# Kernel optimization log

Measured on AMD Instinct MI355X. Metric: run time of the kernel, lower is better.

The kernel has to match this reference:

```python
import jax, jax.numpy as jnp
import numpy as np

E = 256
H = 8
DK = E // H


def setup_inputs() -> dict:
    key = jax.random.key(0)
    ks = jax.random.split(key, 16)
    B, NA, NB = 2, 2048, 2048
    x_a = jax.random.normal(ks[0], (B, NA, E), dtype=jnp.float32)
    x_b = jax.random.normal(ks[1], (B, NB, E), dtype=jnp.float32)
    s = 1.0 / np.sqrt(E)  # kaiming-normal-ish scale
    inp = {"x_a": x_a, "x_b": x_b}
    names = ["wq", "wk_a", "wk_b", "wv_a", "wv_b", "w"]
    for i, n in enumerate(names):
        inp[n + "_w"] = jax.random.normal(ks[2 + 2 * i], (E, E), dtype=jnp.float32) * s
        inp[n + "_b"] = jax.random.normal(ks[3 + 2 * i], (E,), dtype=jnp.float32) * 0.01
    return inp


def _linear(x, w, b):
    # torch nn.Linear: y = x @ w.T + b
    return jnp.einsum('bne,fe->bnf', x, w) + b


def _heads(x):
    # [B, N, E] -> [B, H, N, DK]
    B, N, _ = x.shape
    return x.reshape(B, N, H, DK).transpose(0, 2, 1, 3)


def reference(x_a, x_b, wq_w, wq_b, wk_a_w, wk_a_b, wk_b_w, wk_b_b,
              wv_a_w, wv_a_b, wv_b_w, wv_b_b, w_w, w_b):
    B, NA, _ = x_a.shape
    q = _heads(_linear(x_a, wq_w, wq_b))          # [B,H,NA,DK]
    k_a = _heads(_linear(x_a, wk_a_w, wk_a_b))    # [B,H,NA,DK]
    v_a = _heads(_linear(x_a, wv_a_w, wv_a_b))
    k_b = _heads(_linear(x_b, wk_b_w, wk_b_b))    # [B,H,NB,DK]
    v_b = _heads(_linear(x_b, wv_b_w, wv_b_b))
    k = jnp.concatenate([k_a, k_b], axis=2)       # [B,H,NA+NB,DK]
    v = jnp.concatenate([v_a, v_b], axis=2)
    scores = jnp.einsum('bhqd,bhkd->bhqk', q, k) / jnp.sqrt(jnp.float32(DK))
    p = jax.nn.softmax(scores, axis=-1)           # [B,H,NA,NA+NB]
    z = jnp.einsum('bhqk,bhkd->bhqd', p, v)       # [B,H,NA,DK]
    z = z.transpose(0, 2, 1, 3).reshape(B, NA, E)
    out = _linear(z, w_w, w_b) + x_a
    return out
```

## Files before the change

### kernel.cpp

```cpp
#include <hip/hip_runtime.h>
#include <cstdint>

typedef short bf16x8 __attribute__((ext_vector_type(8)));
typedef float f32x4 __attribute__((ext_vector_type(4)));
typedef unsigned short u16;
typedef unsigned int u32;

#define DEVI static __device__ __forceinline__


DEVI u16 f2bf(float f) {
  u32 x = __builtin_bit_cast(u32, f);
  x += 0x7fffu + ((x >> 16) & 1u);
  return (u16)(x >> 16);
}

DEVI u32 pack_bf2(float lo, float hi) {
  return (u32)f2bf(lo) | ((u32)f2bf(hi) << 16);
}

DEVI u32 cvt_pk_bf16(float lo, float hi) {
  u32 r;
  asm("v_cvt_pk_bf16_f32 %0, %1, %2" : "=v"(r) : "v"(lo), "v"(hi));
  return r;
}

DEVI f32x4 mfma16(bf16x8 a, bf16x8 b, f32x4 c) {
  return __builtin_amdgcn_mfma_f32_16x16x32_bf16(a, b, c, 0, 0, 0);
}

DEVI void load_lds16(const void* g, void* l) {
  __builtin_amdgcn_global_load_lds(
      (const __attribute__((address_space(1))) u32*)g,
      (__attribute__((address_space(3))) u32*)l, 16, 0, 0);
}

#define CSCALE 0.2550351f

DEVI int rho(int k) {
  return ((k >> 5) << 5) | (((k >> 2) & 1) << 4) | (((k >> 3) & 3) << 2) | (k & 3);
}

__global__ __launch_bounds__(256) void convert_kernel(
    const float* __restrict__ xa, const float* __restrict__ xb,
    const float* __restrict__ w0, const float* __restrict__ w1,
    const float* __restrict__ w2, const float* __restrict__ w3,
    const float* __restrict__ w4, const float* __restrict__ w5,
    u16* __restrict__ dst) {
  int i = (int)(blockIdx.x * 256u + threadIdx.x) * 8;
  const float* s;
  if (i < 1048576) {
    s = xa + i;
  } else if (i < 2097152) {
    s = xb + (i - 1048576);
  } else {
    int t = i - 2097152;
    int j = t >> 16, o = t & 65535;
    s = (j == 0 ? w0 : j == 1 ? w1 : j == 2 ? w2 : j == 3 ? w3 : j == 4 ? w4 : w5) + o;
  }
  float4 a = *(const float4*)s;
  float4 b = *(const float4*)(s + 4);
  uint4 o4;
  o4.x = pack_bf2(a.x, a.y);
  o4.y = pack_bf2(a.z, a.w);
  o4.z = pack_bf2(b.x, b.y);
  o4.w = pack_bf2(b.z, b.w);
  *(uint4*)(dst + i) = o4;
}

__global__ __launch_bounds__(256) void proj_kernel(
    const u16* __restrict__ xa_bf, const u16* __restrict__ xb_bf,
    const u16* __restrict__ wbase,
    const float* __restrict__ b0, const float* __restrict__ b1,
    const float* __restrict__ b2, const float* __restrict__ b3,
    const float* __restrict__ b4,
    u16* __restrict__ Qo, u16* __restrict__ Ko, u16* __restrict__ Vo) {
  int job = blockIdx.z;
  const u16* A = (job <= 2) ? xa_bf : xb_bf;
  const u16* W = wbase + job * 65536;
  const float* bias = job == 0 ? b0 : job == 1 ? b1 : job == 2 ? b2 : job == 3 ? b3 : b4;
  int mode = (job == 0) ? 0 : (job == 1 || job == 3) ? 1 : 2;
  int soff = (job >= 3) ? 2048 : 0;

  int tid = threadIdx.x, wid = tid >> 6, lane = tid & 63, g = lane >> 4, c = lane & 15;
  int m0 = blockIdx.x * 64, n0 = blockIdx.y * 64;
  const u16* Ap = A + (size_t)(m0 + wid * 16 + c) * 256 + g * 8;
  const u16* Wp = W + (n0 + c) * 256 + g * 8;
  f32x4 acc[4] = {};
#pragma unroll
  for (int kk = 0; kk < 256; kk += 32) {
    bf16x8 af = *(const bf16x8*)(Ap + kk);
#pragma unroll
    for (int nt = 0; nt < 4; ++nt) {
      bf16x8 bfr = *(const bf16x8*)(Wp + nt * 4096 + kk);
      acc[nt] = mfma16(af, bfr, acc[nt]);
    }
  }
#pragma unroll
  for (int nt = 0; nt < 4; ++nt) {
    int f = n0 + nt * 16 + c;
    float bv = bias[f];
    int h = f >> 5, d = f & 31;
#pragma unroll
    for (int r = 0; r < 4; ++r) {
      int m = m0 + wid * 16 + g * 4 + r;
      int bq = m >> 11, n = m & 2047;
      int bh = bq * 8 + h;
      float y = acc[nt][r] + bv;
      if (mode == 0) {
        Qo[((size_t)bh * 2048 + n) * 32 + d] = f2bf(y * CSCALE);
      } else if (mode == 1) {
        int nk = soff + n;
        int pr = (nk & ~63) | rho(nk & 63);
        Ko[((size_t)bh * 4096 + pr) * 32 + d] = f2bf(y);
      } else {
        int nk = soff + n;
        Vo[(size_t)bh * 131072 + (nk >> 6) * 2048 + ((nk >> 3) & 7) * 256 +
           d * 8 + (nk & 7)] = f2bf(y);
      }
    }
  }
}

__global__ __launch_bounds__(256) void attn_kernel(
    const u16* __restrict__ Q, const u16* __restrict__ K,
    const u16* __restrict__ Vt, float* __restrict__ Zp, float* __restrict__ S) {
  __shared__ __align__(16) unsigned char sbuf[24576];
  int bid = blockIdx.x;
  int xcd = bid & 7, slot = bid >> 3;
  int bh = (xcd << 1) | (slot & 1);
  int rem = slot >> 1;
  int ks = rem & 3, qi = rem >> 2;
  int tid = threadIdx.x, wid = tid >> 6, lane = tid & 63;
  int g = lane >> 4, c = lane & 15;
  int qbase = qi * 256 + wid * 64;

  const unsigned char* Kb =
      (const unsigned char*)K + (size_t)bh * 262144 + (size_t)ks * 65536;
  const unsigned char* Vb =
      (const unsigned char*)Vt + (size_t)bh * 262144 + (size_t)ks * 65536;

  const u16* Qp = Q + ((size_t)bh * 2048 + qbase + c) * 32 + g * 8;
  bf16x8 qf0 = *(const bf16x8*)(Qp);
  bf16x8 qf1 = *(const bf16x8*)(Qp + 16 * 32);
  bf16x8 qf2 = *(const bf16x8*)(Qp + 32 * 32);
  bf16x8 qf3 = *(const bf16x8*)(Qp + 48 * 32);

  int kaddr = c * 64 + ((g ^ ((c >> 1) & 3)) << 4);
  int vaddr = g * 512 + c * 16;

  int o = wid * 1024 + (lane << 4);
  int ko_src = o ^ (((o >> 7) & 3) << 4);

  const u32 one2 = 0x3F803F80u;
  union { u32 u[4]; bf16x8 v; } ones;
  ones.u[0] = one2; ones.u[1] = one2; ones.u[2] = one2; ones.u[3] = one2;

  f32x4 z00 = {}, z01 = {}, z10 = {}, z11 = {};
  f32x4 z20 = {}, z21 = {}, z30 = {}, z31 = {};
  f32x4 zs0 = {}, zs1 = {}, zs2 = {}, zs3 = {};

  load_lds16(Kb + ko_src, sbuf + wid * 1024);
  load_lds16(Vb + o, sbuf + 12288 + wid * 1024);

  int cur = 0;
  for (int t = 0; t < 16; ++t) {
    int nxt = cur + 1;
    if (nxt == 3) nxt = 0;
    if (t + 1 < 16) {
      load_lds16(Kb + (t + 1) * 4096 + ko_src, sbuf + nxt * 4096 + wid * 1024);
      load_lds16(Vb + (t + 1) * 4096 + o, sbuf + 12288 + nxt * 4096 + wid * 1024);
      __builtin_amdgcn_sched_barrier(0);
      asm volatile("s_waitcnt vmcnt(2)" ::: "memory");
    } else {
      __builtin_amdgcn_sched_barrier(0);
      asm volatile("s_waitcnt vmcnt(0)" ::: "memory");
    }
    __builtin_amdgcn_s_barrier();
    __builtin_amdgcn_sched_barrier(0);

    const unsigned char* kbuf = sbuf + cur * 4096;
    const unsigned char* vbuf = sbuf + 12288 + cur * 4096;

    bf16x8 kf0 = *(const bf16x8*)(kbuf + kaddr);
    bf16x8 kf1 = *(const bf16x8*)(kbuf + kaddr + 1024);
    bf16x8 kf2 = *(const bf16x8*)(kbuf + kaddr + 2048);
    bf16x8 kf3 = *(const bf16x8*)(kbuf + kaddr + 3072);
    bf16x8 vf00 = *(const bf16x8*)(vbuf + vaddr);
    bf16x8 vf01 = *(const bf16x8*)(vbuf + vaddr + 2048);
    bf16x8 vf10 = *(const bf16x8*)(vbuf + vaddr + 256);
    bf16x8 vf11 = *(const bf16x8*)(vbuf + vaddr + 2048 + 256);

#define QFRAG(QF, ZA, ZB, ZS)                                              \
    {                                                                      \
      f32x4 zz = {};                                                       \
      __builtin_amdgcn_s_setprio(1);                                       \
      f32x4 s0 = mfma16(kf0, QF, zz);                                      \
      f32x4 s1 = mfma16(kf1, QF, zz);                                      \
      f32x4 s2 = mfma16(kf2, QF, zz);                                      \
      f32x4 s3 = mfma16(kf3, QF, zz);                                      \
      __builtin_amdgcn_s_setprio(0);                                       \
      float e0[4], e1[4], e2[4], e3[4];                                    \
      _Pragma("unroll")                                                    \
      for (int r = 0; r < 4; ++r) {                                        \
        e0[r] = __builtin_amdgcn_exp2f(s0[r]);                             \
        e1[r] = __builtin_amdgcn_exp2f(s1[r]);                             \
        e2[r] = __builtin_amdgcn_exp2f(s2[r]);                             \
        e3[r] = __builtin_amdgcn_exp2f(s3[r]);                             \
      }                                                                    \
      union { u32 u[4]; bf16x8 v; } A0, A1;                                \
      A0.u[0] = cvt_pk_bf16(e0[0], e0[1]);                                 \
      A0.u[1] = cvt_pk_bf16(e0[2], e0[3]);                                 \
      A0.u[2] = cvt_pk_bf16(e1[0], e1[1]);                                 \
      A0.u[3] = cvt_pk_bf16(e1[2], e1[3]);                                 \
      A1.u[0] = cvt_pk_bf16(e2[0], e2[1]);                                 \
      A1.u[1] = cvt_pk_bf16(e2[2], e2[3]);                                 \
      A1.u[2] = cvt_pk_bf16(e3[0], e3[1]);                                 \
      A1.u[3] = cvt_pk_bf16(e3[2], e3[3]);                                 \
      __builtin_amdgcn_s_setprio(1);                                       \
      ZA = mfma16(A0.v, vf00, ZA);                                         \
      ZA = mfma16(A1.v, vf01, ZA);                                         \
      ZB = mfma16(A0.v, vf10, ZB);                                         \
      ZB = mfma16(A1.v, vf11, ZB);                                         \
      ZS = mfma16(A0.v, ones.v, ZS);                                       \
      ZS = mfma16(A1.v, ones.v, ZS);                                       \
      __builtin_amdgcn_s_setprio(0);                                       \
    }

    QFRAG(qf0, z00, z01, zs0)
    QFRAG(qf1, z10, z11, zs1)
    QFRAG(qf2, z20, z21, zs2)
    QFRAG(qf3, z30, z31, zs3)
#undef QFRAG
    cur = nxt;
  }

  size_t zrow = ((size_t)ks * 16 + bh) * 2048;
#define STORE(J, ZA, ZB, ZS)                                               \
  _Pragma("unroll")                                                        \
  for (int r = 0; r < 4; ++r) {                                            \
    int m = qbase + J * 16 + g * 4 + r;                                    \
    float* zp = Zp + (zrow + m) * 32;                                      \
    zp[c] = ZA[r];                                                         \
    zp[16 + c] = ZB[r];                                                    \
    if (c == 0) S[zrow + m] = ZS[r];                                       \
  }
  STORE(0, z00, z01, zs0)
  STORE(1, z10, z11, zs1)
  STORE(2, z20, z21, zs2)
  STORE(3, z30, z31, zs3)
#undef STORE
}

__global__ __launch_bounds__(256) void out_kernel(
    const float* __restrict__ Zp, const float* __restrict__ S,
    const u16* __restrict__ W, const float* __restrict__ bias,
    const float* __restrict__ resid, float* __restrict__ out) {
  int tid = threadIdx.x, wid = tid >> 6, lane = tid & 63, g = lane >> 4, c = lane & 15;
  int m0 = blockIdx.x * 16;
  int mrow = m0 + c;
  int bq = mrow >> 11, n = mrow & 2047;
  const u16* Wp = W + (size_t)(wid * 64 + c) * 256 + g * 8;

  f32x4 acc[4] = {};
#pragma unroll
  for (int h = 0; h < 8; ++h) {
    int bh = bq * 8 + h;
    size_t sb = (size_t)bh * 2048 + n;
    float ts = (S[sb] + S[sb + 32768]) + (S[sb + 65536] + S[sb + 98304]);
    float iv = 1.0f / ts;
    const float* zp = Zp + sb * 32 + g * 8;
    float4 a0 = *(const float4*)zp;
    float4 a1 = *(const float4*)(zp + 4);
    float4 b0 = *(const float4*)(zp + 1048576);
    float4 b1 = *(const float4*)(zp + 1048576 + 4);
    float4 c0 = *(const float4*)(zp + 2097152);
    float4 c1 = *(const float4*)(zp + 2097152 + 4);
    float4 d0 = *(const float4*)(zp + 3145728);
    float4 d1 = *(const float4*)(zp + 3145728 + 4);
    float e0 = ((a0.x + b0.x) + (c0.x + d0.x)) * iv;
    float e1 = ((a0.y + b0.y) + (c0.y + d0.y)) * iv;
    float e2 = ((a0.z + b0.z) + (c0.z + d0.z)) * iv;
    float e3 = ((a0.w + b0.w) + (c0.w + d0.w)) * iv;
    float e4 = ((a1.x + b1.x) + (c1.x + d1.x)) * iv;
    float e5 = ((a1.y + b1.y) + (c1.y + d1.y)) * iv;
    float e6 = ((a1.z + b1.z) + (c1.z + d1.z)) * iv;
    float e7 = ((a1.w + b1.w) + (c1.w + d1.w)) * iv;
    union { u32 u[4]; bf16x8 v; } af;
    af.u[0] = cvt_pk_bf16(e0, e1);
    af.u[1] = cvt_pk_bf16(e2, e3);
    af.u[2] = cvt_pk_bf16(e4, e5);
    af.u[3] = cvt_pk_bf16(e6, e7);
#pragma unroll
    for (int nt = 0; nt < 4; ++nt) {
      bf16x8 bfr = *(const bf16x8*)(Wp + nt * 4096 + h * 32);
      acc[nt] = mfma16(af.v, bfr, acc[nt]);
    }
  }
#pragma unroll
  for (int nt = 0; nt < 4; ++nt) {
    int f = wid * 64 + nt * 16 + c;
    float bv = bias[f];
#pragma unroll
    for (int r = 0; r < 4; ++r) {
      int m = m0 + g * 4 + r;
      out[(size_t)m * 256 + f] = acc[nt][r] + bv + resid[(size_t)m * 256 + f];
    }
  }
}

extern "C" void kernel_launch(void* const* d_in, const int* in_sizes, int n_in,
                              void* d_out, int out_size, void* d_ws, size_t ws_size,
                              hipStream_t stream) {
  const float* xa = (const float*)d_in[0];
  const float* xb = (const float*)d_in[1];
  const float* wq_w = (const float*)d_in[2];
  const float* wq_b = (const float*)d_in[3];
  const float* wka_w = (const float*)d_in[4];
  const float* wka_b = (const float*)d_in[5];
  const float* wkb_w = (const float*)d_in[6];
  const float* wkb_b = (const float*)d_in[7];
  const float* wva_w = (const float*)d_in[8];
  const float* wva_b = (const float*)d_in[9];
  const float* wvb_w = (const float*)d_in[10];
  const float* wvb_b = (const float*)d_in[11];
  const float* w_w = (const float*)d_in[12];
  const float* w_b = (const float*)d_in[13];

  u16* ws = (u16*)d_ws;
  u16* xa_bf = ws;
  u16* xb_bf = ws + 1048576;
  u16* wbf = ws + 2097152;
  u16* Qb = ws + 2490368;
  u16* Kb = ws + 3538944;
  u16* Vtb = ws + 5636096;
  float* Zp = (float*)(ws + 7733248);
  float* S = Zp + 4194304;

  convert_kernel<<<1216, 256, 0, stream>>>(xa, xb, wq_w, wka_w, wva_w, wkb_w,
                                           wvb_w, w_w, ws);
  proj_kernel<<<dim3(64, 4, 5), 256, 0, stream>>>(
      xa_bf, xb_bf, wbf, wq_b, wka_b, wva_b, wkb_b, wvb_b, Qb, Kb, Vtb);
  attn_kernel<<<512, 256, 0, stream>>>(Qb, Kb, Vtb, Zp, S);
  out_kernel<<<256, 256, 0, stream>>>(Zp, S, wbf + 5 * 65536, w_b, xa,
                                      (float*)d_out);
}
```

Baseline: 79.49 us.

## Load K/V fragments directly from global with register double-buffering, drop LDS staging

The attention kernel no longer stages K and V tiles through LDS with async global-to-LDS loads and barriers. Each lane now loads its MFMA fragments straight from global memory into two alternating register sets, which removes block-level synchronisation. V is stored in a plain transposed [bh, d, n] layout. The projection kernel swaps MFMA operand order so Q/K/V outputs are written as packed 4-element bf16 stores instead of scalar ones. The cost is more VGPRs and reliance on L2/L1 for K/V reuse across the four waves of a block, which now each read the same data independently.

Measured after the change: 79.22 us. About the same (-0.3%).

```diff
diff --git a/kernel.cpp b/kernel.cpp
--- a/kernel.cpp
+++ b/kernel.cpp
@@ -27,12 +27,6 @@
 
 DEVI f32x4 mfma16(bf16x8 a, bf16x8 b, f32x4 c) {
   return __builtin_amdgcn_mfma_f32_16x16x32_bf16(a, b, c, 0, 0, 0);
-}
-
-DEVI void load_lds16(const void* g, void* l) {
-  __builtin_amdgcn_global_load_lds(
-      (const __attribute__((address_space(1))) u32*)g,
-      (__attribute__((address_space(3))) u32*)l, 16, 0, 0);
 }
 
 #define CSCALE 0.2550351f
@@ -87,45 +81,77 @@
   const u16* Ap = A + (size_t)(m0 + wid * 16 + c) * 256 + g * 8;
   const u16* Wp = W + (n0 + c) * 256 + g * 8;
   f32x4 acc[4] = {};
-#pragma unroll
-  for (int kk = 0; kk < 256; kk += 32) {
-    bf16x8 af = *(const bf16x8*)(Ap + kk);
+  if (mode == 2) {
+#pragma unroll
+    for (int kk = 0; kk < 256; kk += 32) {
+      bf16x8 af = *(const bf16x8*)(Ap + kk);
+#pragma unroll
+      for (int nt = 0; nt < 4; ++nt) {
+        bf16x8 bfr = *(const bf16x8*)(Wp + nt * 4096 + kk);
+        acc[nt] = mfma16(af, bfr, acc[nt]);
+      }
+    }
+  } else {
+#pragma unroll
+    for (int kk = 0; kk < 256; kk += 32) {
+      bf16x8 af = *(const bf16x8*)(Ap + kk);
+#pragma unroll
+      for (int nt = 0; nt < 4; ++nt) {
+        bf16x8 bfr = *(const bf16x8*)(Wp + nt * 4096 + kk);
+        acc[nt] = mfma16(bfr, af, acc[nt]);
+      }
+    }
+  }
+
+  if (mode == 2) {
+    int mb = m0 + wid * 16 + g * 4;
+    int bq = mb >> 11;
+    int nk = soff + (mb & 2047);
 #pragma unroll
     for (int nt = 0; nt < 4; ++nt) {
-      bf16x8 bfr = *(const bf16x8*)(Wp + nt * 4096 + kk);
-      acc[nt] = mfma16(af, bfr, acc[nt]);
-    }
-  }
-#pragma unroll
-  for (int nt = 0; nt < 4; ++nt) {
-    int f = n0 + nt * 16 + c;
-    float bv = bias[f];
-    int h = f >> 5, d = f & 31;
-#pragma unroll
-    for (int r = 0; r < 4; ++r) {
-      int m = m0 + wid * 16 + g * 4 + r;
-      int bq = m >> 11, n = m & 2047;
+      int f = n0 + nt * 16 + c;
+      int h = f >> 5, d = f & 31;
+      float bv = bias[f];
       int bh = bq * 8 + h;
-      float y = acc[nt][r] + bv;
+      uint2 pw;
+      pw.x = pack_bf2(acc[nt][0] + bv, acc[nt][1] + bv);
+      pw.y = pack_bf2(acc[nt][2] + bv, acc[nt][3] + bv);
+      *(uint2*)(Vo + (size_t)(bh * 32 + d) * 4096 + nk) = pw;
+    }
+  } else {
+    int m = m0 + wid * 16 + c;
+    int bq = m >> 11, n = m & 2047;
+#pragma unroll
+    for (int nt = 0; nt < 4; ++nt) {
+      int fb = n0 + nt * 16 + g * 4;
+      int h = fb >> 5, db = fb & 31;
+      int bh = bq * 8 + h;
+      float4 bv4 = *(const float4*)(bias + fb);
+      float v0 = acc[nt][0] + bv4.x;
+      float v1 = acc[nt][1] + bv4.y;
+      float v2 = acc[nt][2] + bv4.z;
+      float v3 = acc[nt][3] + bv4.w;
+      uint2 pw;
+      u16* dst;
       if (mode == 0) {
-        Qo[((size_t)bh * 2048 + n) * 32 + d] = f2bf(y * CSCALE);
-      } else if (mode == 1) {
+        pw.x = pack_bf2(v0 * CSCALE, v1 * CSCALE);
+        pw.y = pack_bf2(v2 * CSCALE, v3 * CSCALE);
+        dst = Qo + ((size_t)bh * 2048 + n) * 32 + db;
+      } else {
         int nk = soff + n;
         int pr = (nk & ~63) | rho(nk & 63);
-        Ko[((size_t)bh * 4096 + pr) * 32 + d] = f2bf(y);
-      } else {
-        int nk = soff + n;
-        Vo[(size_t)bh * 131072 + (nk >> 6) * 2048 + ((nk >> 3) & 7) * 256 +
-           d * 8 + (nk & 7)] = f2bf(y);
+        pw.x = pack_bf2(v0, v1);
+        pw.y = pack_bf2(v2, v3);
+        dst = Ko + ((size_t)bh * 4096 + pr) * 32 + db;
       }
+      *(uint2*)dst = pw;
     }
   }
 }
 
 __global__ __launch_bounds__(256) void attn_kernel(
     const u16* __restrict__ Q, const u16* __restrict__ K,
-    const u16* __restrict__ Vt, float* __restrict__ Zp, float* __restrict__ S) {
-  __shared__ __align__(16) unsigned char sbuf[24576];
+    const u16* __restrict__ V, float* __restrict__ Zp, float* __restrict__ S) {
   int bid = blockIdx.x;
   int xcd = bid & 7, slot = bid >> 3;
   int bh = (xcd << 1) | (slot & 1);
@@ -135,10 +161,8 @@
   int g = lane >> 4, c = lane & 15;
   int qbase = qi * 256 + wid * 64;
 
-  const unsigned char* Kb =
-      (const unsigned char*)K + (size_t)bh * 262144 + (size_t)ks * 65536;
-  const unsigned char* Vb =
-      (const unsigned char*)Vt + (size_t)bh * 262144 + (size_t)ks * 65536;
+  const u16* Kb = K + (size_t)bh * 131072 + (size_t)ks * 32768;
+  const u16* Vb = V + (size_t)bh * 131072 + (size_t)ks * 1024;
 
   const u16* Qp = Q + ((size_t)bh * 2048 + qbase + c) * 32 + g * 8;
   bf16x8 qf0 = *(const bf16x8*)(Qp);
@@ -146,11 +170,8 @@
   bf16x8 qf2 = *(const bf16x8*)(Qp + 32 * 32);
   bf16x8 qf3 = *(const bf16x8*)(Qp + 48 * 32);
 
-  int kaddr = c * 64 + ((g ^ ((c >> 1) & 3)) << 4);
-  int vaddr = g * 512 + c * 16;
-
-  int o = wid * 1024 + (lane << 4);
-  int ko_src = o ^ (((o >> 7) & 3) << 4);
+  int koff = c * 32 + g * 8;
+  size_t voff = (size_t)c * 4096 + g * 8;
 
   const u32 one2 = 0x3F803F80u;
   union { u32 u[4]; bf16x8 v; } ones;
@@ -160,45 +181,27 @@
   f32x4 z20 = {}, z21 = {}, z30 = {}, z31 = {};
   f32x4 zs0 = {}, zs1 = {}, zs2 = {}, zs3 = {};
 
-  load_lds16(Kb + ko_src, sbuf + wid * 1024);
-  load_lds16(Vb + o, sbuf + 12288 + wid * 1024);
-
-  int cur = 0;
-  for (int t = 0; t < 16; ++t) {
-    int nxt = cur + 1;
-    if (nxt == 3) nxt = 0;
-    if (t + 1 < 16) {
-      load_lds16(Kb + (t + 1) * 4096 + ko_src, sbuf + nxt * 4096 + wid * 1024);
-      load_lds16(Vb + (t + 1) * 4096 + o, sbuf + 12288 + nxt * 4096 + wid * 1024);
-      __builtin_amdgcn_sched_barrier(0);
-      asm volatile("s_waitcnt vmcnt(2)" ::: "memory");
-    } else {
-      __builtin_amdgcn_sched_barrier(0);
-      asm volatile("s_waitcnt vmcnt(0)" ::: "memory");
-    }
-    __builtin_amdgcn_s_barrier();
-    __builtin_amdgcn_sched_barrier(0);
-
-    const unsigned char* kbuf = sbuf + cur * 4096;
-    const unsigned char* vbuf = sbuf + 12288 + cur * 4096;
-
-    bf16x8 kf0 = *(const bf16x8*)(kbuf + kaddr);
-    bf16x8 kf1 = *(const bf16x8*)(kbuf + kaddr + 1024);
-    bf16x8 kf2 = *(const bf16x8*)(kbuf + kaddr + 2048);
-    bf16x8 kf3 = *(const bf16x8*)(kbuf + kaddr + 3072);
-    bf16x8 vf00 = *(const bf16x8*)(vbuf + vaddr);
-    bf16x8 vf01 = *(const bf16x8*)(vbuf + vaddr + 2048);
-    bf16x8 vf10 = *(const bf16x8*)(vbuf + vaddr + 256);
-    bf16x8 vf11 = *(const bf16x8*)(vbuf + vaddr + 2048 + 256);
-
-#define QFRAG(QF, ZA, ZB, ZS)                                              \
+  bf16x8 ka0, ka1, ka2, ka3, va00, va01, va10, va11;
+  bf16x8 kb0, kb1, kb2, kb3, vb00, vb01, vb10, vb11;
+
+#define LOADT(T, K0, K1, K2, K3, V00, V01, V10, V11)                        \
+  K0 = *(const bf16x8*)(Kb + (T) * 2048 + koff);                            \
+  K1 = *(const bf16x8*)(Kb + (T) * 2048 + 512 + koff);                      \
+  K2 = *(const bf16x8*)(Kb + (T) * 2048 + 1024 + koff);                     \
+  K3 = *(const bf16x8*)(Kb + (T) * 2048 + 1536 + koff);                     \
+  V00 = *(const bf16x8*)(Vb + voff + (T) * 64);                             \
+  V01 = *(const bf16x8*)(Vb + voff + (T) * 64 + 32);                        \
+  V10 = *(const bf16x8*)(Vb + voff + 65536 + (T) * 64);                     \
+  V11 = *(const bf16x8*)(Vb + voff + 65536 + (T) * 64 + 32);
+
+#define QFRAG(QF, KF0, KF1, KF2, KF3, VF00, VF01, VF10, VF11, ZA, ZB, ZS)  \
     {                                                                      \
       f32x4 zz = {};                                                       \
       __builtin_amdgcn_s_setprio(1);                                       \
-      f32x4 s0 = mfma16(kf0, QF, zz);                                      \
-      f32x4 s1 = mfma16(kf1, QF, zz);                                      \
-      f32x4 s2 = mfma16(kf2, QF, zz);                                      \
-      f32x4 s3 = mfma16(kf3, QF, zz);                                      \
+      f32x4 s0 = mfma16(KF0, QF, zz);                                      \
+      f32x4 s1 = mfma16(KF1, QF, zz);                                      \
+      f32x4 s2 = mfma16(KF2, QF, zz);                                      \
+      f32x4 s3 = mfma16(KF3, QF, zz);                                      \
       __builtin_amdgcn_s_setprio(0);                                       \
       float e0[4], e1[4], e2[4], e3[4];                                    \
       _Pragma("unroll")                                                    \
@@ -218,22 +221,34 @@
       A1.u[2] = cvt_pk_bf16(e3[0], e3[1]);                                 \
       A1.u[3] = cvt_pk_bf16(e3[2], e3[3]);                                 \
       __builtin_amdgcn_s_setprio(1);                                       \
-      ZA = mfma16(A0.v, vf00, ZA);                                         \
-      ZA = mfma16(A1.v, vf01, ZA);                                         \
-      ZB = mfma16(A0.v, vf10, ZB);                                         \
-      ZB = mfma16(A1.v, vf11, ZB);                                         \
+      ZA = mfma16(A0.v, VF00, ZA);                                         \
+      ZA = mfma16(A1.v, VF01, ZA);                                         \
+      ZB = mfma16(A0.v, VF10, ZB);                                         \
+      ZB = mfma16(A1.v, VF11, ZB);                                         \
       ZS = mfma16(A0.v, ones.v, ZS);                                       \
       ZS = mfma16(A1.v, ones.v, ZS);                                       \
       __builtin_amdgcn_s_setprio(0);                                       \
     }
 
-    QFRAG(qf0, z00, z01, zs0)
-    QFRAG(qf1, z10, z11, zs1)
-    QFRAG(qf2, z20, z21, zs2)
-    QFRAG(qf3, z30, z31, zs3)
+#define COMPUTE(K0, K1, K2, K3, V00, V01, V10, V11)                        \
+    QFRAG(qf0, K0, K1, K2, K3, V00, V01, V10, V11, z00, z01, zs0)          \
+    QFRAG(qf1, K0, K1, K2, K3, V00, V01, V10, V11, z10, z11, zs1)          \
+    QFRAG(qf2, K0, K1, K2, K3, V00, V01, V10, V11, z20, z21, zs2)          \
+    QFRAG(qf3, K0, K1, K2, K3, V00, V01, V10, V11, z30, z31, zs3)
+
+  LOADT(0, ka0, ka1, ka2, ka3, va00, va01, va10, va11)
+  for (int tt = 0; tt < 8; ++tt) {
+    int t = tt * 2;
+    LOADT(t + 1, kb0, kb1, kb2, kb3, vb00, vb01, vb10, vb11)
+    COMPUTE(ka0, ka1, ka2, ka3, va00, va01, va10, va11)
+    if (tt < 7) {
+      LOADT(t + 2, ka0, ka1, ka2, ka3, va00, va01, va10, va11)
+    }
+    COMPUTE(kb0, kb1, kb2, kb3, vb00, vb01, vb10, vb11)
+  }
+#undef COMPUTE
 #undef QFRAG
-    cur = nxt;
-  }
+#undef LOADT
 
   size_t zrow = ((size_t)ks * 16 + bh) * 2048;
 #define STORE(J, ZA, ZB, ZS)                                               \
@@ -333,15 +348,15 @@
   u16* wbf = ws + 2097152;
   u16* Qb = ws + 2490368;
   u16* Kb = ws + 3538944;
-  u16* Vtb = ws + 5636096;
+  u16* Vb = ws + 5636096;
   float* Zp = (float*)(ws + 7733248);
   float* S = Zp + 4194304;
 
   convert_kernel<<<1216, 256, 0, stream>>>(xa, xb, wq_w, wka_w, wva_w, wkb_w,
                                            wvb_w, w_w, ws);
   proj_kernel<<<dim3(64, 4, 5), 256, 0, stream>>>(
-      xa_bf, xb_bf, wbf, wq_b, wka_b, wva_b, wkb_b, wvb_b, Qb, Kb, Vtb);
-  attn_kernel<<<512, 256, 0, stream>>>(Qb, Kb, Vtb, Zp, S);
+      xa_bf, xb_bf, wbf, wq_b, wka_b, wva_b, wkb_b, wvb_b, Qb, Kb, Vb);
+  attn_kernel<<<512, 256, 0, stream>>>(Qb, Kb, Vb, Zp, S);
   out_kernel<<<256, 256, 0, stream>>>(Zp, S, wbf + 5 * 65536, w_b, xa,
                                       (float*)d_out);
 }
```
